# Optimization experiments

Hardware: AMD Instinct MI355X
Metric: run time of the kernel (lower is better)

## Reference

```python
import jax, jax.numpy as jnp
import numpy as np

DN = ('NCHW', 'OIHW', 'NCHW')
COMMITMENT_COST = 0.25


def conv(x, w, b=None, stride=1, pad=0, groups=1):
    o = jax.lax.conv_general_dilated(x, w, (stride, stride), [(pad, pad), (pad, pad)],
                                     feature_group_count=groups, dimension_numbers=DN)
    return o if b is None else o + b[None, :, None, None]


def conv_t(x, w, b=None, stride=2, pad=1, groups=1):
    # w is in torch ConvTranspose2d layout: (in_ch, out_ch//groups, kH, kW)
    in_ch, outg, kh, kw = w.shape
    wf = jnp.flip(w, (-2, -1)).reshape(groups, in_ch // groups, outg, kh, kw)
    wf = wf.transpose(0, 2, 1, 3, 4).reshape(groups * outg, in_ch // groups, kh, kw)
    p = kh - 1 - pad
    o = jax.lax.conv_general_dilated(x, wf, (1, 1), [(p, p), (p, p)],
                                     lhs_dilation=(stride, stride),
                                     feature_group_count=groups, dimension_numbers=DN)
    return o if b is None else o + b[None, :, None, None]


def res_stack(x, w1, w2):
    # w1: (L, nrh, nh//2, 3, 3), w2: (L, nh, nrh//2, 1, 1); groups=2, no bias
    for i in range(w1.shape[0]):
        h = conv(jax.nn.relu(x), w1[i], pad=1, groups=2)
        h = conv(jax.nn.relu(h), w2[i], groups=2)
        x = x + h
    return jax.nn.relu(x)


def vq(z, emb, beta):
    # z: (B, C, H, W); emb: (K, C). EMA updates skipped (eval mode).
    zp = jnp.transpose(z, (0, 2, 3, 1))  # BHWC
    C = emb.shape[1]
    flat = zp.reshape(-1, C)
    d = (jnp.sum(flat ** 2, axis=1, keepdims=True)
         + jnp.sum(emb ** 2, axis=1) - 2.0 * flat @ emb.T)
    idx = jnp.argmin(d, axis=1)
    q = emb[idx].reshape(zp.shape)
    loss = beta * jnp.mean((jax.lax.stop_gradient(q) - zp) ** 2)
    q_st = zp + jax.lax.stop_gradient(q - zp)  # straight-through
    avg = jnp.mean(jax.nn.one_hot(idx, emb.shape[0], dtype=z.dtype), axis=0)
    perplexity = jnp.exp(-jnp.sum(avg * jnp.log(avg + 1e-10)))
    return loss, jnp.transpose(q_st, (0, 3, 1, 2)), perplexity


def _forward(x, eb_dw, eb_db, eb_rw, eb_rb, eb_c1w, eb_c1b, eb_c2w, eb_c2b, eb_c3w, eb_c3b,
             eb_rw1, eb_rw2, et_c1w, et_c1b, et_c2w, et_c2b, et_rw1, et_rw2,
             pvt_w, pvt_b, up_w, up_b, pvb_w, pvb_b, emb_t, emb_b,
             db_c1w, db_c1b, db_rw1, db_rw2, db_t1w, db_t1b, db_t2w, db_t2b,
             db_odw, db_odb, db_orw, db_orb):
    NH = eb_c3w.shape[0]
    ED = emb_t.shape[1]
    # --- EncoderBot ---
    xd = conv(x[:, :1], eb_dw, eb_db)      # depth 1x1 -> NH/4
    xr = conv(x[:, 1:], eb_rw, eb_rb)      # rgb 1x1 -> NH/4
    h = jax.nn.relu(jnp.concatenate([xd, xr], axis=1))
    h = jax.nn.relu(conv(h, eb_c1w, eb_c1b, stride=2, pad=1, groups=2))
    h = jax.nn.relu(conv(h, eb_c2w, eb_c2b, stride=2, pad=1, groups=2))
    h = conv(h, eb_c3w, eb_c3b, pad=1, groups=2)
    enc_b = res_stack(h, eb_rw1, eb_rw2)   # (B, NH, H/4, W/4)
    # --- EncoderTop ---
    t = jax.nn.relu(conv(enc_b, et_c1w, et_c1b, stride=2, pad=1, groups=2))
    t = jax.nn.relu(conv(t, et_c2w, et_c2b, pad=1, groups=2))
    enc_t = res_stack(t, et_rw1, et_rw2)   # (B, NH, H/8, W/8)
    # --- top VQ ---
    zt = conv(enc_t, pvt_w, pvt_b, groups=2)
    loss_t, q_t, perp_t = vq(zt, emb_t, COMMITMENT_COST)
    up_t = conv_t(q_t, up_w, up_b, stride=2, pad=1, groups=2)  # (B, ED, H/4, W/4)
    # --- PreVQBot: regroup channels as (enc_b_d, up_t_d, enc_b_rgb, up_t_rgb) ---
    joined = jnp.concatenate([enc_b[:, :NH // 2], up_t[:, :ED // 2],
                              enc_b[:, NH // 2:], up_t[:, ED // 2:]], axis=1)
    zb = conv(joined, pvb_w, pvb_b, groups=2)
    loss_b, q_b, perp_b = vq(zb, emb_b, COMMITMENT_COST)
    # --- DecoderBot: input cat(up_t, q_b), regrouped (t_d, b_d, t_rgb, b_rgb) ---
    dj = jnp.concatenate([up_t[:, :ED // 2], q_b[:, :ED // 2],
                          up_t[:, ED // 2:], q_b[:, ED // 2:]], axis=1)
    y = conv(dj, db_c1w, db_c1b, pad=1, groups=2)
    y = res_stack(y, db_rw1, db_rw2)
    y = jax.nn.relu(conv_t(y, db_t1w, db_t1b, stride=2, pad=1, groups=2))
    y = conv_t(y, db_t2w, db_t2b, stride=2, pad=1, groups=2)  # (B, NH/4, H, W), no relu
    c = y.shape[1]
    out_d = conv(y[:, :c // 2], db_odw, db_odb)
    out_rgb = conv(y[:, c // 2:], db_orw, db_orb)
    recon = jnp.concatenate([out_d, out_rgb], axis=1)  # (B, 4, H, W)
    return loss_b, loss_t, recon, q_t, q_b


def setup_inputs() -> dict:
    key = jax.random.key(0)
    NH, NRH, L, ED, K = 128, 64, 2, 128, 2048
    B, H, W = 8, 256, 256
    ks = iter(jax.random.split(key, 64))
    def w(*shape):
        return jax.random.normal(next(ks), shape, jnp.float32) * 0.05
    return dict(
        x=jax.random.normal(next(ks), (B, 4, H, W), jnp.float32),
        eb_dw=w(NH // 4, 1, 1, 1), eb_db=w(NH // 4),
        eb_rw=w(NH // 4, 3, 1, 1), eb_rb=w(NH // 4),
        eb_c1w=w(NH // 2, NH // 4, 4, 4), eb_c1b=w(NH // 2),
        eb_c2w=w(NH, NH // 4, 4, 4), eb_c2b=w(NH),
        eb_c3w=w(NH, NH // 2, 3, 3), eb_c3b=w(NH),
        eb_rw1=w(L, NRH, NH // 2, 3, 3), eb_rw2=w(L, NH, NRH // 2, 1, 1),
        et_c1w=w(NH, NH // 2, 4, 4), et_c1b=w(NH),
        et_c2w=w(NH, NH // 2, 3, 3), et_c2b=w(NH),
        et_rw1=w(L, NRH, NH // 2, 3, 3), et_rw2=w(L, NH, NRH // 2, 1, 1),
        pvt_w=w(ED, NH // 2, 1, 1), pvt_b=w(ED),
        up_w=w(ED, ED // 2, 4, 4), up_b=w(ED),
        pvb_w=w(ED, (NH + ED) // 2, 1, 1), pvb_b=w(ED),
        emb_t=jax.random.normal(next(ks), (K, ED), jnp.float32),
        emb_b=jax.random.normal(next(ks), (K, ED), jnp.float32),
        db_c1w=w(NH, ED, 3, 3), db_c1b=w(NH),
        db_rw1=w(L, NRH, NH // 2, 3, 3), db_rw2=w(L, NH, NRH // 2, 1, 1),
        db_t1w=w(NH, NH // 4, 4, 4), db_t1b=w(NH // 2),
        db_t2w=w(NH // 2, NH // 8, 4, 4), db_t2b=w(NH // 4),
        db_odw=w(1, NH // 8, 1, 1), db_odb=w(1),
        db_orw=w(3, NH // 8, 1, 1), db_orb=w(3),
    )


def reference(x, eb_dw, eb_db, eb_rw, eb_rb, eb_c1w, eb_c1b, eb_c2w, eb_c2b, eb_c3w, eb_c3b,
              eb_rw1, eb_rw2, et_c1w, et_c1b, et_c2w, et_c2b, et_rw1, et_rw2,
              pvt_w, pvt_b, up_w, up_b, pvb_w, pvb_b, emb_t, emb_b,
              db_c1w, db_c1b, db_rw1, db_rw2, db_t1w, db_t1b, db_t2w, db_t2b,
              db_odw, db_odb, db_orw, db_orb):
    return _forward(x, eb_dw, eb_db, eb_rw, eb_rb, eb_c1w, eb_c1b, eb_c2w, eb_c2b,
                    eb_c3w, eb_c3b, eb_rw1, eb_rw2, et_c1w, et_c1b, et_c2w, et_c2b,
                    et_rw1, et_rw2, pvt_w, pvt_b, up_w, up_b, pvb_w, pvb_b, emb_t, emb_b,
                    db_c1w, db_c1b, db_rw1, db_rw2, db_t1w, db_t1b, db_t2w, db_t2b,
                    db_odw, db_odb, db_orw, db_orb)
```

## Files before the change

kernel.cpp:

```cpp
#include <hip/hip_runtime.h>
#include <cstddef>

#define TPB 256

__device__ __forceinline__ float4 relu4(float4 v) {
    v.x = fmaxf(v.x, 0.0f); v.y = fmaxf(v.y, 0.0f);
    v.z = fmaxf(v.z, 0.0f); v.w = fmaxf(v.w, 0.0f);
    return v;
}

__device__ __forceinline__ const float* pick_src(const float* a, const float* b,
                                                 int n, int g, int l, int HW) {
    return (l < 64) ? a + ((size_t)n * 128 + g * 64 + l) * HW
                    : b + ((size_t)n * 128 + g * 64 + (l - 64)) * HW;
}

template<int W, int ROWS, bool RELU_IN, bool SPLIT>
__global__ __launch_bounds__(256) void conv3_kernel(
    const float* __restrict__ in, const float* __restrict__ in2,
    const float* __restrict__ wgt, const float* __restrict__ bias,
    float* __restrict__ out, int Cin, int Cout, int relu_out)
{
    constexpr int J = ROWS * W / 64;
    constexpr int ICB = 8;
    constexpr int IN_H = ROWS + 2, IN_W2 = W + 8;
    constexpr int W4 = W / 4;
    __shared__ float s_in[ICB][IN_H][IN_W2];
    __shared__ float s_w[ICB * 9 * 32];

    const int tid = threadIdx.x;
    const int tx = tid & 63, ty = tid >> 6;
    const int n = blockIdx.z, oc0 = blockIdx.y * 32, r0 = blockIdx.x * ROWS;
    const int icg = Cin >> 1, ocg = Cout >> 1;
    const int g = oc0 / ocg;

    float acc[8][J];
    #pragma unroll
    for (int o = 0; o < 8; ++o) {
        const float b = bias ? bias[oc0 + ty * 8 + o] : 0.0f;
        #pragma unroll
        for (int j = 0; j < J; ++j) acc[o][j] = b;
    }

    const float* inb = SPLIT ? nullptr
                             : in + ((size_t)n * Cin + (size_t)g * icg) * (W * W);

    for (int ic0 = 0; ic0 < icg; ic0 += ICB) {
        __syncthreads();
        for (int i = tid; i < ICB * IN_H * W4; i += 256) {
            const int icl = i / (IN_H * W4);
            const int rem = i - icl * (IN_H * W4);
            const int rr = rem / W4, c4 = rem - rr * W4;
            const int y = r0 - 1 + rr;
            float4 v = make_float4(0.f, 0.f, 0.f, 0.f);
            if ((unsigned)y < (unsigned)W) {
                const float* src = SPLIT ? pick_src(in, in2, n, g, ic0 + icl, W * W)
                                         : inb + (size_t)(ic0 + icl) * (W * W);
                v = *(const float4*)(src + (size_t)y * W + 4 * c4);
            }
            if (RELU_IN) v = relu4(v);
            *(float4*)&s_in[icl][rr][4 + 4 * c4] = v;
        }
        for (int i = tid; i < ICB * IN_H; i += 256) {
            const int icl = i / IN_H, rr = i - icl * IN_H;
            s_in[icl][rr][3] = 0.0f;
            s_in[icl][rr][W + 4] = 0.0f;
        }
        for (int i = tid; i < ICB * 9 * 32; i += 256) {
            const int ocl = i & 31, rest = i >> 5;
            const int k = rest % 9, icl = rest / 9;
            s_w[i] = wgt[((size_t)(oc0 + ocl) * icg + (ic0 + icl)) * 9 + k];
        }
        __syncthreads();

        #pragma unroll 1
        for (int icl = 0; icl < ICB; ++icl) {
            const float* swb = s_w + icl * 288 + ty * 8;
            #pragma unroll
            for (int ky = 0; ky < 3; ++ky) {
                #pragma unroll
                for (int kx = 0; kx < 3; ++kx) {
                    const int kq = ky * 3 + kx;
                    const float4 wA = *(const float4*)(swb + kq * 32);
                    const float4 wB = *(const float4*)(swb + kq * 32 + 4);
                    #pragma unroll
                    for (int j = 0; j < J; ++j) {
                        const int p = j * 64 + tx;
                        const int rr = p / W, cc = p - rr * W;
                        const float v = s_in[icl][rr + ky][cc + 3 + kx];
                        acc[0][j] = fmaf(wA.x, v, acc[0][j]);
                        acc[1][j] = fmaf(wA.y, v, acc[1][j]);
                        acc[2][j] = fmaf(wA.z, v, acc[2][j]);
                        acc[3][j] = fmaf(wA.w, v, acc[3][j]);
                        acc[4][j] = fmaf(wB.x, v, acc[4][j]);
                        acc[5][j] = fmaf(wB.y, v, acc[5][j]);
                        acc[6][j] = fmaf(wB.z, v, acc[6][j]);
                        acc[7][j] = fmaf(wB.w, v, acc[7][j]);
                    }
                }
            }
        }
    }

    const int HWo = W * W;
    float* ob = out + ((size_t)n * Cout + oc0 + ty * 8) * HWo;
    #pragma unroll
    for (int o = 0; o < 8; ++o) {
        #pragma unroll
        for (int j = 0; j < J; ++j) {
            const int p = j * 64 + tx;
            const int rr = p / W, cc = p - rr * W;
            float r = acc[o][j];
            if (relu_out) r = fmaxf(r, 0.0f);
            ob[(size_t)o * HWo + (size_t)(r0 + rr) * W + cc] = r;
        }
    }
}

template<int W, int ROWS>
__global__ __launch_bounds__(256) void conv4s2_kernel(
    const float* __restrict__ in, const float* __restrict__ wgt,
    const float* __restrict__ bias, float* __restrict__ out,
    int Cin, int Cout, int relu_out)
{
    constexpr int J = ROWS * W / 64;
    constexpr int ICB = 4;
    constexpr int IN_H = 2 * ROWS + 2, IN_W2 = 2 * W + 8;
    constexpr int W24 = W / 2;
    __shared__ float s_in[ICB][IN_H][IN_W2];
    __shared__ float s_w[ICB * 16 * 32];

    const int tid = threadIdx.x;
    const int tx = tid & 63, ty = tid >> 6;
    const int n = blockIdx.z, oc0 = blockIdx.y * 32, r0 = blockIdx.x * ROWS;
    const int icg = Cin >> 1, ocg = Cout >> 1;
    const int g = oc0 / ocg;
    const int Hin = 2 * W;

    float acc[8][J];
    #pragma unroll
    for (int o = 0; o < 8; ++o) {
        const float b = bias ? bias[oc0 + ty * 8 + o] : 0.0f;
        #pragma unroll
        for (int j = 0; j < J; ++j) acc[o][j] = b;
    }

    const float* inb = in + ((size_t)n * Cin + (size_t)g * icg) * (Hin * Hin);
    for (int ic0 = 0; ic0 < icg; ic0 += ICB) {
        __syncthreads();
        for (int i = tid; i < ICB * IN_H * W24; i += 256) {
            const int icl = i / (IN_H * W24);
            const int rem = i - icl * (IN_H * W24);
            const int rr = rem / W24, c4 = rem - rr * W24;
            const int y = 2 * r0 - 1 + rr;
            float4 v = make_float4(0.f, 0.f, 0.f, 0.f);
            if ((unsigned)y < (unsigned)Hin)
                v = *(const float4*)(inb + (size_t)(ic0 + icl) * (Hin * Hin)
                                     + (size_t)y * Hin + 4 * c4);
            *(float4*)&s_in[icl][rr][4 + 4 * c4] = v;
        }
        for (int i = tid; i < ICB * IN_H; i += 256) {
            const int icl = i / IN_H, rr = i - icl * IN_H;
            s_in[icl][rr][3] = 0.0f;
            s_in[icl][rr][2 * W + 4] = 0.0f;
        }
        for (int i = tid; i < ICB * 16 * 32; i += 256) {
            const int ocl = i & 31, rest = i >> 5;
            const int k = rest & 15, icl = rest >> 4;
            s_w[i] = wgt[((size_t)(oc0 + ocl) * icg + (ic0 + icl)) * 16 + k];
        }
        __syncthreads();

        #pragma unroll 1
        for (int icl = 0; icl < ICB; ++icl) {
            const float* swb = s_w + icl * 512 + ty * 8;
            #pragma unroll
            for (int ky = 0; ky < 4; ++ky) {
                #pragma unroll
                for (int kx = 0; kx < 4; ++kx) {
                    const int kq = ky * 4 + kx;
                    const float4 wA = *(const float4*)(swb + kq * 32);
                    const float4 wB = *(const float4*)(swb + kq * 32 + 4);
                    #pragma unroll
                    for (int j = 0; j < J; ++j) {
                        const int p = j * 64 + tx;
                        const int rr = p / W, cc = p - rr * W;
                        const float v = s_in[icl][2 * rr + ky][2 * cc + 3 + kx];
                        acc[0][j] = fmaf(wA.x, v, acc[0][j]);
                        acc[1][j] = fmaf(wA.y, v, acc[1][j]);
                        acc[2][j] = fmaf(wA.z, v, acc[2][j]);
                        acc[3][j] = fmaf(wA.w, v, acc[3][j]);
                        acc[4][j] = fmaf(wB.x, v, acc[4][j]);
                        acc[5][j] = fmaf(wB.y, v, acc[5][j]);
                        acc[6][j] = fmaf(wB.z, v, acc[6][j]);
                        acc[7][j] = fmaf(wB.w, v, acc[7][j]);
                    }
                }
            }
        }
    }

    const int HWo = W * W;
    float* ob = out + ((size_t)n * Cout + oc0 + ty * 8) * HWo;
    #pragma unroll
    for (int o = 0; o < 8; ++o) {
        #pragma unroll
        for (int j = 0; j < J; ++j) {
            const int p = j * 64 + tx;
            const int rr = p / W, cc = p - rr * W;
            float r = acc[o][j];
            if (relu_out) r = fmaxf(r, 0.0f);
            ob[(size_t)o * HWo + (size_t)(r0 + rr) * W + cc] = r;
        }
    }
}

template<bool RELU_IN, bool ACC, bool RELU_OUT, bool SPLIT>
__global__ __launch_bounds__(256) void conv1_kernel(
    const float* __restrict__ in, const float* __restrict__ in2,
    const float* __restrict__ wgt, const float* __restrict__ bias,
    float* __restrict__ out, int Cin, int Cout, int HW)
{
    constexpr int ICB = 16;
    __shared__ float s_in[ICB][128];
    __shared__ float s_w[ICB * 32];

    const int tid = threadIdx.x;
    const int tx = tid & 63, ty = tid >> 6;
    const int n = blockIdx.z, oc0 = blockIdx.y * 32, p0 = blockIdx.x * 128;
    const int icg = Cin >> 1, ocg = Cout >> 1;
    const int g = oc0 / ocg;

    float acc[8][2];
    #pragma unroll
    for (int o = 0; o < 8; ++o) {
        const float b = bias ? bias[oc0 + ty * 8 + o] : 0.0f;
        acc[o][0] = b; acc[o][1] = b;
    }

    const float* inb = SPLIT ? nullptr
                             : in + ((size_t)n * Cin + (size_t)g * icg) * HW + p0;
    for (int ic0 = 0; ic0 < icg; ic0 += ICB) {
        __syncthreads();
        for (int i = tid; i < ICB * 32; i += 256) {
            const int icl = i >> 5, c4 = i & 31;
            const float* src = SPLIT ? pick_src(in, in2, n, g, ic0 + icl, HW) + p0
                                     : inb + (size_t)(ic0 + icl) * HW;
            float4 v = *(const float4*)(src + 4 * c4);
            if (RELU_IN) v = relu4(v);
            *(float4*)&s_in[icl][4 * c4] = v;
        }
        for (int i = tid; i < ICB * 32; i += 256) {
            const int ocl = i & 31, icl = i >> 5;
            s_w[i] = wgt[(size_t)(oc0 + ocl) * icg + ic0 + icl];
        }
        __syncthreads();

        #pragma unroll 4
        for (int icl = 0; icl < ICB; ++icl) {
            const float4 wA = *(const float4*)(s_w + icl * 32 + ty * 8);
            const float4 wB = *(const float4*)(s_w + icl * 32 + ty * 8 + 4);
            #pragma unroll
            for (int j = 0; j < 2; ++j) {
                const float v = s_in[icl][j * 64 + tx];
                acc[0][j] = fmaf(wA.x, v, acc[0][j]);
                acc[1][j] = fmaf(wA.y, v, acc[1][j]);
                acc[2][j] = fmaf(wA.z, v, acc[2][j]);
                acc[3][j] = fmaf(wA.w, v, acc[3][j]);
                acc[4][j] = fmaf(wB.x, v, acc[4][j]);
                acc[5][j] = fmaf(wB.y, v, acc[5][j]);
                acc[6][j] = fmaf(wB.z, v, acc[6][j]);
                acc[7][j] = fmaf(wB.w, v, acc[7][j]);
            }
        }
    }

    float* ob = out + ((size_t)n * Cout + oc0 + ty * 8) * HW + p0;
    #pragma unroll
    for (int o = 0; o < 8; ++o) {
        #pragma unroll
        for (int j = 0; j < 2; ++j) {
            const size_t idx = (size_t)o * HW + j * 64 + tx;
            float r = acc[o][j];
            if (ACC) r += ob[idx];
            if (RELU_OUT) r = fmaxf(r, 0.0f);
            ob[idx] = r;
        }
    }
}

template<int W, int ROWS, int OCT>
__global__ __launch_bounds__(64 * (OCT / 8)) void convt4_kernel(
    const float* __restrict__ in, const float* __restrict__ wgt,
    const float* __restrict__ bias, float* __restrict__ out,
    int Cin, int Cout, int relu_out)
{
    constexpr int NTHR = 64 * (OCT / 8);
    constexpr int PXT  = ROWS * W / 64;
    constexpr int WP   = W / 64;
    constexpr int ICB  = 8;
    constexpr int RIN  = ((ROWS + 1) >> 1) + 2;
    constexpr int CIN  = W / 2 + 2;
    __shared__ float s_in[ICB][RIN][CIN];
    __shared__ float s_w[ICB * 16 * OCT];

    const int tid = threadIdx.x;
    const int tx = tid & 63, ty = tid >> 6;
    const int n = blockIdx.z;
    const int oc0 = blockIdx.y * OCT;
    const int r0 = blockIdx.x * ROWS;
    const int icg = Cin >> 1, ocg = Cout >> 1;
    const int g = oc0 / ocg, of0 = oc0 - g * ocg;
    const int Hin = W / 2;
    const int iy_lo = (r0 - 2) >> 1;

    float acc[8][PXT];
    #pragma unroll
    for (int o = 0; o < 8; ++o) {
        const float b = bias ? bias[oc0 + ty * 8 + o] : 0.0f;
        #pragma unroll
        for (int j = 0; j < PXT; ++j) acc[o][j] = b;
    }

    const float* inb = in + ((size_t)n * Cin + (size_t)g * icg) * (Hin * Hin);
    const int kxl = ((tx + 1) & 1);
    const int hx  = (tx + 1) >> 1;

    for (int ic0 = 0; ic0 < icg; ic0 += ICB) {
        __syncthreads();
        for (int i = tid; i < ICB * RIN * CIN; i += NTHR) {
            const int icl = i / (RIN * CIN);
            const int rem = i - icl * (RIN * CIN);
            const int rr = rem / CIN, cc = rem - rr * CIN;
            const int y = iy_lo + rr, x = cc - 1;
            float v = 0.0f;
            if ((unsigned)y < (unsigned)Hin && (unsigned)x < (unsigned)Hin)
                v = inb[(size_t)(ic0 + icl) * (Hin * Hin) + y * Hin + x];
            s_in[icl][rr][cc] = v;
        }
        for (int i = tid; i < ICB * 16 * OCT; i += NTHR) {
            const int ocl = i & (OCT - 1);
            const int rest = i / OCT;
            const int k = rest & 15, icl = rest >> 4;
            s_w[i] = wgt[((size_t)(g * icg + ic0 + icl) * ocg + of0 + ocl) * 16 + k];
        }
        __syncthreads();

        #pragma unroll 1
        for (int icl = 0; icl < ICB; ++icl) {
            const float* swb = s_w + icl * 16 * OCT + ty * 8;
            #pragma unroll
            for (int tt = 0; tt < 4; ++tt) {
                const int ty2 = tt >> 1, tx2 = tt & 1;
                float4 wp0[2], wp1[2];
                #pragma unroll
                for (int par = 0; par < 2; ++par) {
                    const int koff = ((2 * ty2 + par) * 4 + (kxl + 2 * tx2)) * OCT;
                    wp0[par] = *(const float4*)(swb + koff);
                    wp1[par] = *(const float4*)(swb + koff + 4);
                }
                const int cbase = hx - tx2 + 1;
                #pragma unroll
                for (int j = 0; j < PXT; ++j) {
                    const int row_j = j / WP, m_j = j - row_j * WP;
                    const int pj = (row_j + 1) & 1;
                    const int rloc = (row_j + 1 - pj) / 2 - ty2 + 1;
                    const float v = s_in[icl][rloc][32 * m_j + cbase];
                    const float4 wa = pj ? wp0[1] : wp0[0];
                    const float4 wb = pj ? wp1[1] : wp1[0];
                    acc[0][j] = fmaf(wa.x, v, acc[0][j]);
                    acc[1][j] = fmaf(wa.y, v, acc[1][j]);
                    acc[2][j] = fmaf(wa.z, v, acc[2][j]);
                    acc[3][j] = fmaf(wa.w, v, acc[3][j]);
                    acc[4][j] = fmaf(wb.x, v, acc[4][j]);
                    acc[5][j] = fmaf(wb.y, v, acc[5][j]);
                    acc[6][j] = fmaf(wb.z, v, acc[6][j]);
                    acc[7][j] = fmaf(wb.w, v, acc[7][j]);
                }
            }
        }
    }

    const int HWo = W * W;
    float* ob = out + ((size_t)n * Cout + oc0 + ty * 8) * HWo;
    #pragma unroll
    for (int o = 0; o < 8; ++o) {
        #pragma unroll
        for (int j = 0; j < PXT; ++j) {
            const int row_j = j / WP, m_j = j - row_j * WP;
            float r = acc[o][j];
            if (relu_out) r = fmaxf(r, 0.0f);
            ob[(size_t)o * HWo + (size_t)(r0 + row_j) * W + 64 * m_j + tx] = r;
        }
    }
}

__global__ void head_kernel(const float* __restrict__ x,
                            const float* __restrict__ dw, const float* __restrict__ db,
                            const float* __restrict__ rw, const float* __restrict__ rb,
                            float* __restrict__ out)
{
    const int idx = blockIdx.x * TPB + threadIdx.x;
    const int HW4 = 16384;
    if (idx >= 8 * 64 * HW4) return;
    const int p4 = idx & (HW4 - 1);
    const int t = idx >> 14;
    const int c = t & 63, n = t >> 6;
    const float4* xb4 = (const float4*)(x + (size_t)n * 4 * 65536);
    float4 v;
    if (c < 32) {
        const float w = dw[c], b = db[c];
        const float4 d = xb4[p4];
        v.x = fmaf(d.x, w, b); v.y = fmaf(d.y, w, b);
        v.z = fmaf(d.z, w, b); v.w = fmaf(d.w, w, b);
    } else {
        const int cc = c - 32;
        const float w0 = rw[cc * 3], w1 = rw[cc * 3 + 1], w2 = rw[cc * 3 + 2];
        const float b = rb[cc];
        const float4 r = xb4[HW4 + p4], g4 = xb4[2 * HW4 + p4], bl = xb4[3 * HW4 + p4];
        v.x = fmaf(bl.x, w2, fmaf(g4.x, w1, fmaf(r.x, w0, b)));
        v.y = fmaf(bl.y, w2, fmaf(g4.y, w1, fmaf(r.y, w0, b)));
        v.z = fmaf(bl.z, w2, fmaf(g4.z, w1, fmaf(r.z, w0, b)));
        v.w = fmaf(bl.w, w2, fmaf(g4.w, w1, fmaf(r.w, w0, b)));
    }
    ((float4*)out)[idx] = relu4(v);
}

__global__ void emb_norm_kernel(const float* __restrict__ emb, float* __restrict__ en, int K)
{
    const int k = blockIdx.x * TPB + threadIdx.x;
    if (k >= K) return;
    const float4* e = (const float4*)(emb + (size_t)k * 128);
    float s = 0.0f;
    for (int c = 0; c < 32; ++c) {
        const float4 t = e[c];
        s = fmaf(t.x, t.x, s); s = fmaf(t.y, t.y, s);
        s = fmaf(t.z, t.z, s); s = fmaf(t.w, t.w, s);
    }
    en[k] = s;
}

#define VQ_TV 64
#define VQ_TE 64
__global__ __launch_bounds__(256) void vq_kernel(
    const float* __restrict__ z, const float* __restrict__ emb,
    const float* __restrict__ en_g,
    float* __restrict__ q, float* __restrict__ lossp,
    int HW, int Kc)
{
    __shared__ float zs[32][65][4];
    __shared__ float es[32][65][4];
    __shared__ float en[VQ_TE];
    __shared__ float rdd[VQ_TV][16];
    __shared__ int   rdi[VQ_TV][16];
    __shared__ int   idxv[VQ_TV];
    __shared__ float red[256];

    const int tid = threadIdx.x;
    const int vg = tid >> 4, eg = tid & 15;
    const long long gv0 = (long long)blockIdx.x * VQ_TV;
    const int n = (int)(gv0 / HW);
    const int p0 = (int)(gv0 - (long long)n * HW);
    const float* zb = z + (size_t)n * 128 * HW + p0;

    for (int i = tid; i < 64 * 128; i += 256) {
        const int v = i & 63, c = i >> 6;
        zs[c >> 2][v][c & 3] = zb[(size_t)c * HW + v];
    }
    __syncthreads();

    float best[4]; int bidx[4];
    #pragma unroll
    for (int r = 0; r < 4; ++r) { best[r] = 1e30f; bidx[r] = 0; }

    for (int e0 = 0; e0 < Kc; e0 += VQ_TE) {
        for (int i = tid; i < VQ_TE * 128; i += 256) {
            const int c = i & 127, el = i >> 7;
            es[c >> 2][el][c & 3] = emb[(size_t)(e0 + el) * 128 + c];
        }
        if (tid < VQ_TE) en[tid] = en_g[e0 + tid];
        __syncthreads();

        float dot[4][4];
        #pragma unroll
        for (int r = 0; r < 4; ++r)
            #pragma unroll
            for (int s = 0; s < 4; ++s) dot[r][s] = 0.0f;

        for (int c4 = 0; c4 < 32; ++c4) {
            float4 zr[4], ee[4];
            #pragma unroll
            for (int r = 0; r < 4; ++r) zr[r] = *(const float4*)&zs[c4][4 * vg + r][0];
            #pragma unroll
            for (int s = 0; s < 4; ++s) ee[s] = *(const float4*)&es[c4][eg + 16 * s][0];
            #pragma unroll
            for (int r = 0; r < 4; ++r) {
                #pragma unroll
                for (int s = 0; s < 4; ++s) {
                    dot[r][s] = fmaf(zr[r].x, ee[s].x, dot[r][s]);
                    dot[r][s] = fmaf(zr[r].y, ee[s].y, dot[r][s]);
                    dot[r][s] = fmaf(zr[r].z, ee[s].z, dot[r][s]);
                    dot[r][s] = fmaf(zr[r].w, ee[s].w, dot[r][s]);
                }
            }
        }
        #pragma unroll
        for (int s = 0; s < 4; ++s) {
            const float e2 = en[eg + 16 * s];
            const int ei = e0 + eg + 16 * s;
            #pragma unroll
            for (int r = 0; r < 4; ++r) {
                const float d = e2 - 2.0f * dot[r][s];
                if (d < best[r]) { best[r] = d; bidx[r] = ei; }
            }
        }
        __syncthreads();
    }

    #pragma unroll
    for (int r = 0; r < 4; ++r) { rdd[4 * vg + r][eg] = best[r]; rdi[4 * vg + r][eg] = bidx[r]; }
    __syncthreads();
    if (tid < VQ_TV) {
        float bd = rdd[tid][0]; int bi = rdi[tid][0];
        for (int j = 1; j < 16; ++j) {
            const float d = rdd[tid][j]; const int i2 = rdi[tid][j];
            if (d < bd || (d == bd && i2 < bi)) { bd = d; bi = i2; }
        }
        idxv[tid] = bi;
    }
    __syncthreads();

    float ls = 0.0f;
    float* qb = q + (size_t)n * 128 * HW + p0;
    for (int i = tid; i < 64 * 128; i += 256) {
        const int v = i & 63, c = i >> 6;
        const float e = emb[(size_t)idxv[v] * 128 + c];
        qb[(size_t)c * HW + v] = e;
        const float diff = e - zs[c >> 2][v][c & 3];
        ls = fmaf(diff, diff, ls);
    }
    red[tid] = ls;
    __syncthreads();
    for (int s = 128; s > 0; s >>= 1) {
        if (tid < s) red[tid] += red[tid + s];
        __syncthreads();
    }
    if (tid == 0) lossp[blockIdx.x] = red[0];
}

__global__ void loss_finish_kernel(const float* __restrict__ p, int n, float scale,
                                   float* __restrict__ out)
{
    __shared__ float red[256];
    float s = 0.0f;
    for (int i = threadIdx.x; i < n; i += 256) s += p[i];
    red[threadIdx.x] = s;
    __syncthreads();
    for (int k = 128; k > 0; k >>= 1) {
        if (threadIdx.x < k) red[threadIdx.x] += red[threadIdx.x + k];
        __syncthreads();
    }
    if (threadIdx.x == 0) out[0] = red[0] * scale;
}

__global__ void outconv_kernel(const float* __restrict__ y,
                               const float* __restrict__ odw, const float* __restrict__ odb,
                               const float* __restrict__ orw, const float* __restrict__ orb,
                               float* __restrict__ out)
{
    const int idx = blockIdx.x * TPB + threadIdx.x;
    const int HW4 = 16384;
    if (idx >= 8 * 4 * HW4) return;
    const int p4 = idx & (HW4 - 1);
    const int t = idx >> 14;
    const int c = t & 3, n = t >> 2;
    const float4* yb4 = (const float4*)(y + (size_t)n * 32 * 65536);
    float4 v;
    const int base = (c == 0) ? 0 : 16;
    const float* wv = (c == 0) ? odw : orw + (c - 1) * 16;
    const float b = (c == 0) ? odb[0] : orb[c - 1];
    v.x = b; v.y = b; v.z = b; v.w = b;
    for (int k = 0; k < 16; ++k) {
        const float w = wv[k];
        const float4 f = yb4[(size_t)(base + k) * HW4 + p4];
        v.x = fmaf(f.x, w, v.x); v.y = fmaf(f.y, w, v.y);
        v.z = fmaf(f.z, w, v.z); v.w = fmaf(f.w, w, v.w);
    }
    ((float4*)out)[idx] = v;
}

extern "C" void kernel_launch(void* const* d_in, const int* in_sizes, int n_in,
                              void* d_out, int out_size, void* d_ws, size_t ws_size,
                              hipStream_t stream)
{
    const float* x      = (const float*)d_in[0];
    const float* eb_dw  = (const float*)d_in[1];
    const float* eb_db  = (const float*)d_in[2];
    const float* eb_rw  = (const float*)d_in[3];
    const float* eb_rb  = (const float*)d_in[4];
    const float* eb_c1w = (const float*)d_in[5];
    const float* eb_c1b = (const float*)d_in[6];
    const float* eb_c2w = (const float*)d_in[7];
    const float* eb_c2b = (const float*)d_in[8];
    const float* eb_c3w = (const float*)d_in[9];
    const float* eb_c3b = (const float*)d_in[10];
    const float* eb_rw1 = (const float*)d_in[11];
    const float* eb_rw2 = (const float*)d_in[12];
    const float* et_c1w = (const float*)d_in[13];
    const float* et_c1b = (const float*)d_in[14];
    const float* et_c2w = (const float*)d_in[15];
    const float* et_c2b = (const float*)d_in[16];
    const float* et_rw1 = (const float*)d_in[17];
    const float* et_rw2 = (const float*)d_in[18];
    const float* pvt_w  = (const float*)d_in[19];
    const float* pvt_b  = (const float*)d_in[20];
    const float* up_w   = (const float*)d_in[21];
    const float* up_b   = (const float*)d_in[22];
    const float* pvb_w  = (const float*)d_in[23];
    const float* pvb_b  = (const float*)d_in[24];
    const float* emb_t  = (const float*)d_in[25];
    const float* emb_b  = (const float*)d_in[26];
    const float* db_c1w = (const float*)d_in[27];
    const float* db_c1b = (const float*)d_in[28];
    const float* db_rw1 = (const float*)d_in[29];
    const float* db_rw2 = (const float*)d_in[30];
    const float* db_t1w = (const float*)d_in[31];
    const float* db_t1b = (const float*)d_in[32];
    const float* db_t2w = (const float*)d_in[33];
    const float* db_t2b = (const float*)d_in[34];
    const float* db_odw = (const float*)d_in[35];
    const float* db_odb = (const float*)d_in[36];
    const float* db_orw = (const float*)d_in[37];
    const float* db_orb = (const float*)d_in[38];

    float* ws  = (float*)d_ws;
    float* out = (float*)d_out;

    const size_t OFF_H0   = 0;
    const size_t OFF_H1   = 33554432;
    const size_t OFF_H2   = 0;
    const size_t OFF_ENCB = 4194304;
    const size_t OFF_RH   = 8388608;
    const size_t OFF_T1   = 10485760;
    const size_t OFF_T2   = 11534336;
    const size_t OFF_ZT   = 12582912;
    const size_t OFF_UPT  = 13631488;
    const size_t OFF_ZB   = 17825792;
    const size_t OFF_Y    = 22020096;
    const size_t OFF_Y1   = 26214400;
    const size_t OFF_Y2   = 0;
    const size_t OFF_ENT  = 34603008;
    const size_t OFF_ENB  = 34605056;
    const size_t OFF_LPT  = 34607104;
    const size_t OFF_LPB  = 34607232;
    const size_t NEED     = 41943680;
    if (ws_size < NEED * sizeof(float)) return;

    float* o_loss_b = out + 0;
    float* o_loss_t = out + 1;
    float* o_recon  = out + 2;
    float* o_qt     = out + 2 + 8 * 4 * 65536;
    float* o_qb     = o_qt + 8 * 128 * 1024;

    head_kernel<<<8 * 64 * 16384 / TPB, TPB, 0, stream>>>(
        x, eb_dw, eb_db, eb_rw, eb_rb, ws + OFF_H0);
    conv4s2_kernel<128, 2><<<dim3(64, 2, 8), 256, 0, stream>>>(
        ws + OFF_H0, eb_c1w, eb_c1b, ws + OFF_H1, 64, 64, 1);
    conv4s2_kernel<64, 2><<<dim3(32, 4, 8), 256, 0, stream>>>(
        ws + OFF_H1, eb_c2w, eb_c2b, ws + OFF_H2, 64, 128, 1);
    emb_norm_kernel<<<8, TPB, 0, stream>>>(emb_t, ws + OFF_ENT, 2048);
    emb_norm_kernel<<<8, TPB, 0, stream>>>(emb_b, ws + OFF_ENB, 2048);
    conv3_kernel<64, 2, false, false><<<dim3(32, 4, 8), 256, 0, stream>>>(
        ws + OFF_H2, nullptr, eb_c3w, eb_c3b, ws + OFF_ENCB, 128, 128, 0);
    for (int i = 0; i < 2; ++i) {
        conv3_kernel<64, 2, true, false><<<dim3(32, 2, 8), 256, 0, stream>>>(
            ws + OFF_ENCB, nullptr, eb_rw1 + (size_t)i * 64 * 64 * 9, nullptr,
            ws + OFF_RH, 128, 64, 0);
        if (i == 1)
            conv1_kernel<true, true, true, false><<<dim3(32, 4, 8), 256, 0, stream>>>(
                ws + OFF_RH, nullptr, eb_rw2 + (size_t)i * 128 * 32, nullptr,
                ws + OFF_ENCB, 64, 128, 4096);
        else
            conv1_kernel<true, true, false, false><<<dim3(32, 4, 8), 256, 0, stream>>>(
                ws + OFF_RH, nullptr, eb_rw2 + (size_t)i * 128 * 32, nullptr,
                ws + OFF_ENCB, 64, 128, 4096);
    }

    conv4s2_kernel<32, 2><<<dim3(16, 4, 8), 256, 0, stream>>>(
        ws + OFF_ENCB, et_c1w, et_c1b, ws + OFF_T1, 128, 128, 1);
    conv3_kernel<32, 2, false, false><<<dim3(16, 4, 8), 256, 0, stream>>>(
        ws + OFF_T1, nullptr, et_c2w, et_c2b, ws + OFF_T2, 128, 128, 1);
    for (int i = 0; i < 2; ++i) {
        conv3_kernel<32, 2, true, false><<<dim3(16, 2, 8), 256, 0, stream>>>(
            ws + OFF_T2, nullptr, et_rw1 + (size_t)i * 64 * 64 * 9, nullptr,
            ws + OFF_RH, 128, 64, 0);
        if (i == 1)
            conv1_kernel<true, true, true, false><<<dim3(8, 4, 8), 256, 0, stream>>>(
                ws + OFF_RH, nullptr, et_rw2 + (size_t)i * 128 * 32, nullptr,
                ws + OFF_T2, 64, 128, 1024);
        else
            conv1_kernel<true, true, false, false><<<dim3(8, 4, 8), 256, 0, stream>>>(
                ws + OFF_RH, nullptr, et_rw2 + (size_t)i * 128 * 32, nullptr,
                ws + OFF_T2, 64, 128, 1024);
    }

    conv1_kernel<false, false, false, false><<<dim3(8, 4, 8), 256, 0, stream>>>(
        ws + OFF_T2, nullptr, pvt_w, pvt_b, ws + OFF_ZT, 128, 128, 1024);
    vq_kernel<<<128, 256, 0, stream>>>(ws + OFF_ZT, emb_t, ws + OFF_ENT, o_qt,
                                       ws + OFF_LPT, 1024, 2048);
    loss_finish_kernel<<<1, 256, 0, stream>>>(ws + OFF_LPT, 128,
                                              0.25f / (8192.0f * 128.0f), o_loss_t);

    convt4_kernel<64, 2, 32><<<dim3(32, 4, 8), 256, 0, stream>>>(
        o_qt, up_w, up_b, ws + OFF_UPT, 128, 128, 0);

    conv1_kernel<false, false, false, true><<<dim3(32, 4, 8), 256, 0, stream>>>(
        ws + OFF_ENCB, ws + OFF_UPT, pvb_w, pvb_b, ws + OFF_ZB, 256, 128, 4096);
    vq_kernel<<<512, 256, 0, stream>>>(ws + OFF_ZB, emb_b, ws + OFF_ENB, o_qb,
                                       ws + OFF_LPB, 4096, 2048);
    loss_finish_kernel<<<1, 256, 0, stream>>>(ws + OFF_LPB, 512,
                                              0.25f / (32768.0f * 128.0f), o_loss_b);

    conv3_kernel<64, 2, false, true><<<dim3(32, 4, 8), 256, 0, stream>>>(
        ws + OFF_UPT, o_qb, db_c1w, db_c1b, ws + OFF_Y, 256, 128, 0);
    for (int i = 0; i < 2; ++i) {
        conv3_kernel<64, 2, true, false><<<dim3(32, 2, 8), 256, 0, stream>>>(
            ws + OFF_Y, nullptr, db_rw1 + (size_t)i * 64 * 64 * 9, nullptr,
            ws + OFF_RH, 128, 64, 0);
        if (i == 1)
            conv1_kernel<true, true, true, false><<<dim3(32, 4, 8), 256, 0, stream>>>(
                ws + OFF_RH, nullptr, db_rw2 + (size_t)i * 128 * 32, nullptr,
                ws + OFF_Y, 64, 128, 4096);
        else
            conv1_kernel<true, true, false, false><<<dim3(32, 4, 8), 256, 0, stream>>>(
                ws + OFF_RH, nullptr, db_rw2 + (size_t)i * 128 * 32, nullptr,
                ws + OFF_Y, 64, 128, 4096);
    }
    convt4_kernel<128, 2, 32><<<dim3(64, 2, 8), 256, 0, stream>>>(
        ws + OFF_Y, db_t1w, db_t1b, ws + OFF_Y1, 128, 64, 1);
    convt4_kernel<256, 2, 16><<<dim3(128, 2, 8), 128, 0, stream>>>(
        ws + OFF_Y1, db_t2w, db_t2b, ws + OFF_Y2, 64, 32, 0);
    outconv_kernel<<<8 * 4 * 16384 / TPB, TPB, 0, stream>>>(
        ws + OFF_Y2, db_odw, db_odb, db_orw, db_orb, o_recon);
}
```

Measured before the change: 1.799 ms.

## Register-block conv3, conv1 and VQ kernels with larger per-thread tiles

The 3x3 conv kernel now gives each thread four adjacent output columns. It loads a sliding window of eight inputs per row so that neighbouring taps reuse registers, and it writes outputs as float4. The 1x1 conv kernel moves to 64 output channels by 256 pixels per block, with a 16x4 register tile per thread. The VQ kernel uses 128 vectors per block, an 8x8 dot tile, vectorized loads, and a shuffle-based argmin reduction. Several launch grids are also retuned to larger row tiles. The aim is fewer LDS reads per FMA and better memory coalescing, at the cost of higher register pressure and fewer blocks in flight.

```diff
diff --git a/kernel.cpp b/kernel.cpp
--- a/kernel.cpp
+++ b/kernel.cpp
@@ -15,31 +15,32 @@
                     : b + ((size_t)n * 128 + g * 64 + (l - 64)) * HW;
 }
 
-template<int W, int ROWS, bool RELU_IN, bool SPLIT>
-__global__ __launch_bounds__(256) void conv3_kernel(
+template<int W, bool RELU_IN, bool SPLIT>
+__global__ __launch_bounds__(256) void conv3c_kernel(
     const float* __restrict__ in, const float* __restrict__ in2,
     const float* __restrict__ wgt, const float* __restrict__ bias,
     float* __restrict__ out, int Cin, int Cout, int relu_out)
 {
-    constexpr int J = ROWS * W / 64;
-    constexpr int ICB = 8;
+    constexpr int ROWS = 256 / W;
+    constexpr int CPR  = W / 4;
+    constexpr int ICB  = 8;
     constexpr int IN_H = ROWS + 2, IN_W2 = W + 8;
-    constexpr int W4 = W / 4;
     __shared__ float s_in[ICB][IN_H][IN_W2];
     __shared__ float s_w[ICB * 9 * 32];
 
     const int tid = threadIdx.x;
     const int tx = tid & 63, ty = tid >> 6;
+    const int row = tx / CPR, cg = tx % CPR;
     const int n = blockIdx.z, oc0 = blockIdx.y * 32, r0 = blockIdx.x * ROWS;
     const int icg = Cin >> 1, ocg = Cout >> 1;
     const int g = oc0 / ocg;
 
-    float acc[8][J];
+    float acc[8][4];
     #pragma unroll
     for (int o = 0; o < 8; ++o) {
         const float b = bias ? bias[oc0 + ty * 8 + o] : 0.0f;
         #pragma unroll
-        for (int j = 0; j < J; ++j) acc[o][j] = b;
+        for (int j = 0; j < 4; ++j) acc[o][j] = b;
     }
 
     const float* inb = SPLIT ? nullptr
@@ -47,10 +48,10 @@
 
     for (int ic0 = 0; ic0 < icg; ic0 += ICB) {
         __syncthreads();
-        for (int i = tid; i < ICB * IN_H * W4; i += 256) {
-            const int icl = i / (IN_H * W4);
-            const int rem = i - icl * (IN_H * W4);
-            const int rr = rem / W4, c4 = rem - rr * W4;
+        for (int i = tid; i < ICB * IN_H * CPR; i += 256) {
+            const int icl = i / (IN_H * CPR);
+            const int rem = i - icl * (IN_H * CPR);
+            const int rr = rem / CPR, c4 = rem - rr * CPR;
             const int y = r0 - 1 + rr;
             float4 v = make_float4(0.f, 0.f, 0.f, 0.f);
             if ((unsigned)y < (unsigned)W) {
@@ -59,12 +60,15 @@
                 v = *(const float4*)(src + (size_t)y * W + 4 * c4);
             }
             if (RELU_IN) v = relu4(v);
-            *(float4*)&s_in[icl][rr][4 + 4 * c4] = v;
+            *(float2*)&s_in[icl][rr][2 + 4 * c4] = make_float2(v.x, v.y);
+            *(float2*)&s_in[icl][rr][4 + 4 * c4] = make_float2(v.z, v.w);
         }
         for (int i = tid; i < ICB * IN_H; i += 256) {
             const int icl = i / IN_H, rr = i - icl * IN_H;
-            s_in[icl][rr][3] = 0.0f;
-            s_in[icl][rr][W + 4] = 0.0f;
+            s_in[icl][rr][0] = 0.0f;
+            s_in[icl][rr][1] = 0.0f;
+            s_in[icl][rr][W + 2] = 0.0f;
+            s_in[icl][rr][W + 3] = 0.0f;
         }
         for (int i = tid; i < ICB * 9 * 32; i += 256) {
             const int ocl = i & 31, rest = i >> 5;
@@ -78,16 +82,17 @@
             const float* swb = s_w + icl * 288 + ty * 8;
             #pragma unroll
             for (int ky = 0; ky < 3; ++ky) {
+                const float4 A = *(const float4*)&s_in[icl][row + ky][4 * cg];
+                const float4 B = *(const float4*)&s_in[icl][row + ky][4 * cg + 4];
+                const float win[8] = {A.x, A.y, A.z, A.w, B.x, B.y, B.z, B.w};
                 #pragma unroll
                 for (int kx = 0; kx < 3; ++kx) {
                     const int kq = ky * 3 + kx;
                     const float4 wA = *(const float4*)(swb + kq * 32);
                     const float4 wB = *(const float4*)(swb + kq * 32 + 4);
                     #pragma unroll
-                    for (int j = 0; j < J; ++j) {
-                        const int p = j * 64 + tx;
-                        const int rr = p / W, cc = p - rr * W;
-                        const float v = s_in[icl][rr + ky][cc + 3 + kx];
+                    for (int j = 0; j < 4; ++j) {
+                        const float v = win[j + kx + 1];
                         acc[0][j] = fmaf(wA.x, v, acc[0][j]);
                         acc[1][j] = fmaf(wA.y, v, acc[1][j]);
                         acc[2][j] = fmaf(wA.z, v, acc[2][j]);
@@ -106,14 +111,10 @@
     float* ob = out + ((size_t)n * Cout + oc0 + ty * 8) * HWo;
     #pragma unroll
     for (int o = 0; o < 8; ++o) {
-        #pragma unroll
-        for (int j = 0; j < J; ++j) {
-            const int p = j * 64 + tx;
-            const int rr = p / W, cc = p - rr * W;
-            float r = acc[o][j];
-            if (relu_out) r = fmaxf(r, 0.0f);
-            ob[(size_t)o * HWo + (size_t)(r0 + rr) * W + cc] = r;
-        }
+        float4 r4;
+        r4.x = acc[o][0]; r4.y = acc[o][1]; r4.z = acc[o][2]; r4.w = acc[o][3];
+        if (relu_out) r4 = relu4(r4);
+        *(float4*)&ob[(size_t)o * HWo + (size_t)(r0 + row) * W + 4 * cg] = r4;
     }
 }
 
@@ -216,76 +217,76 @@
 }
 
 template<bool RELU_IN, bool ACC, bool RELU_OUT, bool SPLIT>
-__global__ __launch_bounds__(256) void conv1_kernel(
+__global__ __launch_bounds__(256) void conv1c_kernel(
     const float* __restrict__ in, const float* __restrict__ in2,
     const float* __restrict__ wgt, const float* __restrict__ bias,
     float* __restrict__ out, int Cin, int Cout, int HW)
 {
     constexpr int ICB = 16;
-    __shared__ float s_in[ICB][128];
-    __shared__ float s_w[ICB * 32];
+    __shared__ float s_in[ICB][256];
+    __shared__ float s_w[ICB * 64];
 
     const int tid = threadIdx.x;
     const int tx = tid & 63, ty = tid >> 6;
-    const int n = blockIdx.z, oc0 = blockIdx.y * 32, p0 = blockIdx.x * 128;
+    const int n = blockIdx.z, oc0 = blockIdx.y * 64, p0 = blockIdx.x * 256;
     const int icg = Cin >> 1, ocg = Cout >> 1;
     const int g = oc0 / ocg;
 
-    float acc[8][2];
-    #pragma unroll
-    for (int o = 0; o < 8; ++o) {
-        const float b = bias ? bias[oc0 + ty * 8 + o] : 0.0f;
-        acc[o][0] = b; acc[o][1] = b;
+    float acc[16][4];
+    #pragma unroll
+    for (int o = 0; o < 16; ++o) {
+        const float b = bias ? bias[oc0 + ty * 16 + o] : 0.0f;
+        #pragma unroll
+        for (int j = 0; j < 4; ++j) acc[o][j] = b;
     }
 
     const float* inb = SPLIT ? nullptr
                              : in + ((size_t)n * Cin + (size_t)g * icg) * HW + p0;
     for (int ic0 = 0; ic0 < icg; ic0 += ICB) {
         __syncthreads();
-        for (int i = tid; i < ICB * 32; i += 256) {
-            const int icl = i >> 5, c4 = i & 31;
+        for (int i = tid; i < ICB * 64; i += 256) {
+            const int icl = i >> 6, c4 = i & 63;
             const float* src = SPLIT ? pick_src(in, in2, n, g, ic0 + icl, HW) + p0
                                      : inb + (size_t)(ic0 + icl) * HW;
             float4 v = *(const float4*)(src + 4 * c4);
             if (RELU_IN) v = relu4(v);
             *(float4*)&s_in[icl][4 * c4] = v;
         }
-        for (int i = tid; i < ICB * 32; i += 256) {
-            const int ocl = i & 31, icl = i >> 5;
+        for (int i = tid; i < ICB * 64; i += 256) {
+            const int ocl = i & 63, icl = i >> 6;
             s_w[i] = wgt[(size_t)(oc0 + ocl) * icg + ic0 + icl];
         }
         __syncthreads();
 
-        #pragma unroll 4
+        #pragma unroll 2
         for (int icl = 0; icl < ICB; ++icl) {
-            const float4 wA = *(const float4*)(s_w + icl * 32 + ty * 8);
-            const float4 wB = *(const float4*)(s_w + icl * 32 + ty * 8 + 4);
-            #pragma unroll
-            for (int j = 0; j < 2; ++j) {
-                const float v = s_in[icl][j * 64 + tx];
-                acc[0][j] = fmaf(wA.x, v, acc[0][j]);
-                acc[1][j] = fmaf(wA.y, v, acc[1][j]);
-                acc[2][j] = fmaf(wA.z, v, acc[2][j]);
-                acc[3][j] = fmaf(wA.w, v, acc[3][j]);
-                acc[4][j] = fmaf(wB.x, v, acc[4][j]);
-                acc[5][j] = fmaf(wB.y, v, acc[5][j]);
-                acc[6][j] = fmaf(wB.z, v, acc[6][j]);
-                acc[7][j] = fmaf(wB.w, v, acc[7][j]);
+            const float4 v4 = *(const float4*)&s_in[icl][4 * tx];
+            const float vv[4] = {v4.x, v4.y, v4.z, v4.w};
+            #pragma unroll
+            for (int u = 0; u < 4; ++u) {
+                const float4 w4 = *(const float4*)(s_w + icl * 64 + ty * 16 + 4 * u);
+                #pragma unroll
+                for (int j = 0; j < 4; ++j) {
+                    acc[4 * u + 0][j] = fmaf(w4.x, vv[j], acc[4 * u + 0][j]);
+                    acc[4 * u + 1][j] = fmaf(w4.y, vv[j], acc[4 * u + 1][j]);
+                    acc[4 * u + 2][j] = fmaf(w4.z, vv[j], acc[4 * u + 2][j]);
+                    acc[4 * u + 3][j] = fmaf(w4.w, vv[j], acc[4 * u + 3][j]);
+                }
             }
         }
     }
 
-    float* ob = out + ((size_t)n * Cout + oc0 + ty * 8) * HW + p0;
-    #pragma unroll
-    for (int o = 0; o < 8; ++o) {
-        #pragma unroll
-        for (int j = 0; j < 2; ++j) {
-            const size_t idx = (size_t)o * HW + j * 64 + tx;
-            float r = acc[o][j];
-            if (ACC) r += ob[idx];
-            if (RELU_OUT) r = fmaxf(r, 0.0f);
-            ob[idx] = r;
-        }
+    float* ob = out + ((size_t)n * Cout + oc0 + ty * 16) * HW + p0;
+    #pragma unroll
+    for (int o = 0; o < 16; ++o) {
+        float4 r4;
+        r4.x = acc[o][0]; r4.y = acc[o][1]; r4.z = acc[o][2]; r4.w = acc[o][3];
+        if (ACC) {
+            const float4 prev = *(const float4*)&ob[(size_t)o * HW + 4 * tx];
+            r4.x += prev.x; r4.y += prev.y; r4.z += prev.z; r4.w += prev.w;
+        }
+        if (RELU_OUT) r4 = relu4(r4);
+        *(float4*)&ob[(size_t)o * HW + 4 * tx] = r4;
     }
 }
 
@@ -440,63 +441,66 @@
     en[k] = s;
 }
 
-#define VQ_TV 64
+#define VQ_TV 128
 #define VQ_TE 64
-__global__ __launch_bounds__(256) void vq_kernel(
+__global__ __launch_bounds__(128) void vq_kernel(
     const float* __restrict__ z, const float* __restrict__ emb,
     const float* __restrict__ en_g,
     float* __restrict__ q, float* __restrict__ lossp,
     int HW, int Kc)
 {
-    __shared__ float zs[32][65][4];
+    __shared__ float zs[32][129][4];
     __shared__ float es[32][65][4];
     __shared__ float en[VQ_TE];
-    __shared__ float rdd[VQ_TV][16];
-    __shared__ int   rdi[VQ_TV][16];
     __shared__ int   idxv[VQ_TV];
-    __shared__ float red[256];
+    __shared__ float red[128];
 
     const int tid = threadIdx.x;
-    const int vg = tid >> 4, eg = tid & 15;
+    const int vg = tid >> 3, eg = tid & 7;
     const long long gv0 = (long long)blockIdx.x * VQ_TV;
     const int n = (int)(gv0 / HW);
     const int p0 = (int)(gv0 - (long long)n * HW);
     const float* zb = z + (size_t)n * 128 * HW + p0;
 
-    for (int i = tid; i < 64 * 128; i += 256) {
-        const int v = i & 63, c = i >> 6;
-        zs[c >> 2][v][c & 3] = zb[(size_t)c * HW + v];
+    for (int i = tid; i < 4096; i += 128) {
+        const int c = i >> 5, v4 = i & 31;
+        const float4 v = *(const float4*)(zb + (size_t)c * HW + 4 * v4);
+        zs[c >> 2][4 * v4 + 0][c & 3] = v.x;
+        zs[c >> 2][4 * v4 + 1][c & 3] = v.y;
+        zs[c >> 2][4 * v4 + 2][c & 3] = v.z;
+        zs[c >> 2][4 * v4 + 3][c & 3] = v.w;
     }
     __syncthreads();
 
-    float best[4]; int bidx[4];
-    #pragma unroll
-    for (int r = 0; r < 4; ++r) { best[r] = 1e30f; bidx[r] = 0; }
+    float best[8]; int bidx[8];
+    #pragma unroll
+    for (int r = 0; r < 8; ++r) { best[r] = 1e30f; bidx[r] = 0; }
 
     for (int e0 = 0; e0 < Kc; e0 += VQ_TE) {
-        for (int i = tid; i < VQ_TE * 128; i += 256) {
-            const int c = i & 127, el = i >> 7;
-            es[c >> 2][el][c & 3] = emb[(size_t)(e0 + el) * 128 + c];
+        for (int i = tid; i < 2048; i += 128) {
+            const int e = i >> 5, c4 = i & 31;
+            const float4 v = *(const float4*)(emb + (size_t)(e0 + e) * 128 + 4 * c4);
+            *(float4*)&es[c4][e][0] = v;
         }
         if (tid < VQ_TE) en[tid] = en_g[e0 + tid];
         __syncthreads();
 
-        float dot[4][4];
-        #pragma unroll
-        for (int r = 0; r < 4; ++r)
-            #pragma unroll
-            for (int s = 0; s < 4; ++s) dot[r][s] = 0.0f;
+        float dot[8][8];
+        #pragma unroll
+        for (int r = 0; r < 8; ++r)
+            #pragma unroll
+            for (int s = 0; s < 8; ++s) dot[r][s] = 0.0f;
 
         for (int c4 = 0; c4 < 32; ++c4) {
-            float4 zr[4], ee[4];
-            #pragma unroll
-            for (int r = 0; r < 4; ++r) zr[r] = *(const float4*)&zs[c4][4 * vg + r][0];
-            #pragma unroll
-            for (int s = 0; s < 4; ++s) ee[s] = *(const float4*)&es[c4][eg + 16 * s][0];
-            #pragma unroll
-            for (int r = 0; r < 4; ++r) {
+            float4 zr[8], ee[8];
+            #pragma unroll
+            for (int r = 0; r < 8; ++r) zr[r] = *(const float4*)&zs[c4][vg + 16 * r][0];
+            #pragma unroll
+            for (int s = 0; s < 8; ++s) ee[s] = *(const float4*)&es[c4][eg + 8 * s][0];
+            #pragma unroll
+            for (int r = 0; r < 8; ++r) {
                 #pragma unroll
-                for (int s = 0; s < 4; ++s) {
+                for (int s = 0; s < 8; ++s) {
                     dot[r][s] = fmaf(zr[r].x, ee[s].x, dot[r][s]);
                     dot[r][s] = fmaf(zr[r].y, ee[s].y, dot[r][s]);
                     dot[r][s] = fmaf(zr[r].z, ee[s].z, dot[r][s]);
@@ -505,11 +509,11 @@
             }
         }
         #pragma unroll
-        for (int s = 0; s < 4; ++s) {
-            const float e2 = en[eg + 16 * s];
-            const int ei = e0 + eg + 16 * s;
-            #pragma unroll
-            for (int r = 0; r < 4; ++r) {
+        for (int s = 0; s < 8; ++s) {
+            const float e2 = en[eg + 8 * s];
+            const int ei = e0 + eg + 8 * s;
+            #pragma unroll
+            for (int r = 0; r < 8; ++r) {
                 const float d = e2 - 2.0f * dot[r][s];
                 if (d < best[r]) { best[r] = d; bidx[r] = ei; }
             }
@@ -518,30 +522,42 @@
     }
 
     #pragma unroll
-    for (int r = 0; r < 4; ++r) { rdd[4 * vg + r][eg] = best[r]; rdi[4 * vg + r][eg] = bidx[r]; }
-    __syncthreads();
-    if (tid < VQ_TV) {
-        float bd = rdd[tid][0]; int bi = rdi[tid][0];
-        for (int j = 1; j < 16; ++j) {
-            const float d = rdd[tid][j]; const int i2 = rdi[tid][j];
-            if (d < bd || (d == bd && i2 < bi)) { bd = d; bi = i2; }
-        }
-        idxv[tid] = bi;
+    for (int off = 4; off > 0; off >>= 1) {
+        #pragma unroll
+        for (int r = 0; r < 8; ++r) {
+            const float d2 = __shfl_down(best[r], (unsigned)off, 8);
+            const int   i2 = __shfl_down(bidx[r], (unsigned)off, 8);
+            if (d2 < best[r] || (d2 == best[r] && i2 < bidx[r])) {
+                best[r] = d2; bidx[r] = i2;
+            }
+        }
+    }
+    if (eg == 0) {
+        #pragma unroll
+        for (int r = 0; r < 8; ++r) idxv[vg + 16 * r] = bidx[r];
     }
     __syncthreads();
 
     float ls = 0.0f;
     float* qb = q + (size_t)n * 128 * HW + p0;
-    for (int i = tid; i < 64 * 128; i += 256) {
-        const int v = i & 63, c = i >> 6;
-        const float e = emb[(size_t)idxv[v] * 128 + c];
-        qb[(size_t)c * HW + v] = e;
-        const float diff = e - zs[c >> 2][v][c & 3];
-        ls = fmaf(diff, diff, ls);
+    for (int i = tid; i < 4096; i += 128) {
+        const int c = i >> 5, v4 = i & 31;
+        float4 e4;
+        e4.x = emb[(size_t)idxv[4 * v4 + 0] * 128 + c];
+        e4.y = emb[(size_t)idxv[4 * v4 + 1] * 128 + c];
+        e4.z = emb[(size_t)idxv[4 * v4 + 2] * 128 + c];
+        e4.w = emb[(size_t)idxv[4 * v4 + 3] * 128 + c];
+        *(float4*)(qb + (size_t)c * HW + 4 * v4) = e4;
+        const float d0 = e4.x - zs[c >> 2][4 * v4 + 0][c & 3];
+        const float d1 = e4.y - zs[c >> 2][4 * v4 + 1][c & 3];
+        const float d2 = e4.z - zs[c >> 2][4 * v4 + 2][c & 3];
+        const float d3 = e4.w - zs[c >> 2][4 * v4 + 3][c & 3];
+        ls = fmaf(d0, d0, ls); ls = fmaf(d1, d1, ls);
+        ls = fmaf(d2, d2, ls); ls = fmaf(d3, d3, ls);
     }
     red[tid] = ls;
     __syncthreads();
-    for (int s = 128; s > 0; s >>= 1) {
+    for (int s = 64; s > 0; s >>= 1) {
         if (tid < s) red[tid] += red[tid + s];
         __syncthreads();
     }
@@ -666,73 +682,73 @@
         x, eb_dw, eb_db, eb_rw, eb_rb, ws + OFF_H0);
     conv4s2_kernel<128, 2><<<dim3(64, 2, 8), 256, 0, stream>>>(
         ws + OFF_H0, eb_c1w, eb_c1b, ws + OFF_H1, 64, 64, 1);
-    conv4s2_kernel<64, 2><<<dim3(32, 4, 8), 256, 0, stream>>>(
+    conv4s2_kernel<64, 4><<<dim3(16, 4, 8), 256, 0, stream>>>(
         ws + OFF_H1, eb_c2w, eb_c2b, ws + OFF_H2, 64, 128, 1);
     emb_norm_kernel<<<8, TPB, 0, stream>>>(emb_t, ws + OFF_ENT, 2048);
     emb_norm_kernel<<<8, TPB, 0, stream>>>(emb_b, ws + OFF_ENB, 2048);
-    conv3_kernel<64, 2, false, false><<<dim3(32, 4, 8), 256, 0, stream>>>(
+    conv3c_kernel<64, false, false><<<dim3(16, 4, 8), 256, 0, stream>>>(
         ws + OFF_H2, nullptr, eb_c3w, eb_c3b, ws + OFF_ENCB, 128, 128, 0);
     for (int i = 0; i < 2; ++i) {
-        conv3_kernel<64, 2, true, false><<<dim3(32, 2, 8), 256, 0, stream>>>(
+        conv3c_kernel<64, true, false><<<dim3(16, 2, 8), 256, 0, stream>>>(
             ws + OFF_ENCB, nullptr, eb_rw1 + (size_t)i * 64 * 64 * 9, nullptr,
             ws + OFF_RH, 128, 64, 0);
         if (i == 1)
-            conv1_kernel<true, true, true, false><<<dim3(32, 4, 8), 256, 0, stream>>>(
+            conv1c_kernel<true, true, true, false><<<dim3(16, 2, 8), 256, 0, stream>>>(
                 ws + OFF_RH, nullptr, eb_rw2 + (size_t)i * 128 * 32, nullptr,
                 ws + OFF_ENCB, 64, 128, 4096);
         else
-            conv1_kernel<true, true, false, false><<<dim3(32, 4, 8), 256, 0, stream>>>(
+            conv1c_kernel<true, true, false, false><<<dim3(16, 2, 8), 256, 0, stream>>>(
                 ws + OFF_RH, nullptr, eb_rw2 + (size_t)i * 128 * 32, nullptr,
                 ws + OFF_ENCB, 64, 128, 4096);
     }
 
-    conv4s2_kernel<32, 2><<<dim3(16, 4, 8), 256, 0, stream>>>(
+    conv4s2_kernel<32, 4><<<dim3(8, 4, 8), 256, 0, stream>>>(
         ws + OFF_ENCB, et_c1w, et_c1b, ws + OFF_T1, 128, 128, 1);
-    conv3_kernel<32, 2, false, false><<<dim3(16, 4, 8), 256, 0, stream>>>(
+    conv3c_kernel<32, false, false><<<dim3(4, 4, 8), 256, 0, stream>>>(
         ws + OFF_T1, nullptr, et_c2w, et_c2b, ws + OFF_T2, 128, 128, 1);
     for (int i = 0; i < 2; ++i) {
-        conv3_kernel<32, 2, true, false><<<dim3(16, 2, 8), 256, 0, stream>>>(
+        conv3c_kernel<32, true, false><<<dim3(4, 2, 8), 256, 0, stream>>>(
             ws + OFF_T2, nullptr, et_rw1 + (size_t)i * 64 * 64 * 9, nullptr,
             ws + OFF_RH, 128, 64, 0);
         if (i == 1)
-            conv1_kernel<true, true, true, false><<<dim3(8, 4, 8), 256, 0, stream>>>(
+            conv1c_kernel<true, true, true, false><<<dim3(4, 2, 8), 256, 0, stream>>>(
                 ws + OFF_RH, nullptr, et_rw2 + (size_t)i * 128 * 32, nullptr,
                 ws + OFF_T2, 64, 128, 1024);
         else
-            conv1_kernel<true, true, false, false><<<dim3(8, 4, 8), 256, 0, stream>>>(
+            conv1c_kernel<true, true, false, false><<<dim3(4, 2, 8), 256, 0, stream>>>(
                 ws + OFF_RH, nullptr, et_rw2 + (size_t)i * 128 * 32, nullptr,
                 ws + OFF_T2, 64, 128, 1024);
     }
 
-    conv1_kernel<false, false, false, false><<<dim3(8, 4, 8), 256, 0, stream>>>(
+    conv1c_kernel<false, false, false, false><<<dim3(4, 2, 8), 256, 0, stream>>>(
         ws + OFF_T2, nullptr, pvt_w, pvt_b, ws + OFF_ZT, 128, 128, 1024);
-    vq_kernel<<<128, 256, 0, stream>>>(ws + OFF_ZT, emb_t, ws + OFF_ENT, o_qt,
-                                       ws + OFF_LPT, 1024, 2048);
-    loss_finish_kernel<<<1, 256, 0, stream>>>(ws + OFF_LPT, 128,
+    vq_kernel<<<64, 128, 0, stream>>>(ws + OFF_ZT, emb_t, ws + OFF_ENT, o_qt,
+                                      ws + OFF_LPT, 1024, 2048);
+    loss_finish_kernel<<<1, 256, 0, stream>>>(ws + OFF_LPT, 64,
                                               0.25f / (8192.0f * 128.0f), o_loss_t);
 
-    convt4_kernel<64, 2, 32><<<dim3(32, 4, 8), 256, 0, stream>>>(
+    convt4_kernel<64, 4, 32><<<dim3(16, 4, 8), 256, 0, stream>>>(
         o_qt, up_w, up_b, ws + OFF_UPT, 128, 128, 0);
 
-    conv1_kernel<false, false, false, true><<<dim3(32, 4, 8), 256, 0, stream>>>(
+    conv1c_kernel<false, false, false, true><<<dim3(16, 2, 8), 256, 0, stream>>>(
         ws + OFF_ENCB, ws + OFF_UPT, pvb_w, pvb_b, ws + OFF_ZB, 256, 128, 4096);
-    vq_kernel<<<512, 256, 0, stream>>>(ws + OFF_ZB, emb_b, ws + OFF_ENB, o_qb,
+    vq_kernel<<<256, 128, 0, stream>>>(ws + OFF_ZB, emb_b, ws + OFF_ENB, o_qb,
                                        ws + OFF_LPB, 4096, 2048);
-    loss_finish_kernel<<<1, 256, 0, stream>>>(ws + OFF_LPB, 512,
+    loss_finish_kernel<<<1, 256, 0, stream>>>(ws + OFF_LPB, 256,
                                               0.25f / (32768.0f * 128.0f), o_loss_b);
 
-    conv3_kernel<64, 2, false, true><<<dim3(32, 4, 8), 256, 0, stream>>>(
+    conv3c_kernel<64, false, true><<<dim3(16, 4, 8), 256, 0, stream>>>(
         ws + OFF_UPT, o_qb, db_c1w, db_c1b, ws + OFF_Y, 256, 128, 0);
     for (int i = 0; i < 2; ++i) {
-        conv3_kernel<64, 2, true, false><<<dim3(32, 2, 8), 256, 0, stream>>>(
+        conv3c_kernel<64, true, false><<<dim3(16, 2, 8), 256, 0, stream>>>(
             ws + OFF_Y, nullptr, db_rw1 + (size_t)i * 64 * 64 * 9, nullptr,
             ws + OFF_RH, 128, 64, 0);
         if (i == 1)
-            conv1_kernel<true, true, true, false><<<dim3(32, 4, 8), 256, 0, stream>>>(
+            conv1c_kernel<true, true, true, false><<<dim3(16, 2, 8), 256, 0, stream>>>(
                 ws + OFF_RH, nullptr, db_rw2 + (size_t)i * 128 * 32, nullptr,
                 ws + OFF_Y, 64, 128, 4096);
         else
-            conv1_kernel<true, true, false, false><<<dim3(32, 4, 8), 256, 0, stream>>>(
+            conv1c_kernel<true, true, false, false><<<dim3(16, 2, 8), 256, 0, stream>>>(
                 ws + OFF_RH, nullptr, db_rw2 + (size_t)i * 128 * 32, nullptr,
                 ws + OFF_Y, 64, 128, 4096);
     }
```

Result: slower. 2.664 ms (+48.1%).
